# Performance work log

Hardware: AMD Instinct MI355X
Metric: run time of the kernel (lower is better)

The kernel has to match this reference:

```python
import jax, jax.numpy as jnp
import numpy as np

N = 50000      # nodes
E = 400000     # lower-adjacency edges (avg degree 8)
D = 128        # input_dim == output_dim (o_dim in DEC_HOGNN)
GEO = 20       # geo_dim
H = 3          # heads
C = 128        # out_channels per head
NUM_LAYERS = 3


def _lin_init(key, fan_in, fan_out, extra=()):
    s = 1.0 / np.sqrt(fan_in)
    return jax.random.uniform(key, extra + (fan_in, fan_out), jnp.float32, -s, s)


def setup_inputs() -> dict:
    key = jax.random.key(0)
    ks = jax.random.split(key, 20)
    inp = {
        "h": jax.random.normal(ks[0], (N, D), jnp.float32),
        "lower_adj_feat": jax.random.normal(ks[1], (E, GEO), jnp.float32),
        "dir_w": jax.random.normal(ks[2], (E, 1), jnp.float32),
        "src_idx": jax.random.randint(ks[3], (E,), 0, N),
        "dst_idx": jax.random.randint(ks[4], (E,), 0, N),
        # edge_encoder: Linear(2*D + geo + 1 -> D)
        "W_ee": _lin_init(ks[5], 2 * D + GEO + 1, D),
        "b_ee": jnp.zeros((D,), jnp.float32),
        # residual linear (layer 0 only; others Identity)
        "W_res": _lin_init(ks[6], D, D),
        "b_res": jnp.zeros((D,), jnp.float32),
        # 3 TransformerConv layers, all in=D out=C heads=H (stacked)
        "Wq": _lin_init(ks[7], D, H * C, (NUM_LAYERS,)),
        "bq": jnp.zeros((NUM_LAYERS, H * C), jnp.float32),
        "Wk": _lin_init(ks[8], D, H * C, (NUM_LAYERS,)),
        "bk": jnp.zeros((NUM_LAYERS, H * C), jnp.float32),
        "Wv": _lin_init(ks[9], D, H * C, (NUM_LAYERS,)),
        "bv": jnp.zeros((NUM_LAYERS, H * C), jnp.float32),
        "We": _lin_init(ks[10], D, H * C, (NUM_LAYERS,)),
        "be": jnp.zeros((NUM_LAYERS, H * C), jnp.float32),
        # lin_skip: in -> out_channels (concat=False)
        "Ws": _lin_init(ks[11], D, C, (NUM_LAYERS,)),
        "bs": jnp.zeros((NUM_LAYERS, C), jnp.float32),
        # ctr_lin: Linear(input_dim + output_dim -> output_dim)
        "W_ctr": _lin_init(ks[12], 2 * D, D),
        "b_ctr": jnp.zeros((D,), jnp.float32),
    }
    return inp


def _transformer_conv(x, src, dst, e_attr, Wq, bq, Wk, bk, Wv, bv, We, be, Ws, bs):
    """PyG TransformerConv, heads=H, concat=False (head mean), root skip."""
    n = x.shape[0]
    q = (x @ Wq + bq).reshape(n, H, C)
    k = (x @ Wk + bk).reshape(n, H, C)
    v = (x @ Wv + bv).reshape(n, H, C)
    e = (e_attr @ We + be).reshape(-1, H, C)      # [E,H,C]
    ke = k[src] + e                                # edge-conditioned keys
    alpha = (q[dst] * ke).sum(-1) / jnp.sqrt(jnp.asarray(C, x.dtype))  # [E,H]
    # segment softmax over destination nodes
    amax = jax.ops.segment_max(alpha, dst, num_segments=n)
    amax = jnp.where(jnp.isfinite(amax), amax, 0.0)
    ex = jnp.exp(alpha - amax[dst])
    den = jax.ops.segment_sum(ex, dst, num_segments=n)
    w = ex / (den[dst] + 1e-16)
    msg = (v[src] + e) * w[:, :, None]             # [E,H,C]
    out = jax.ops.segment_sum(msg.reshape(-1, H * C), dst, num_segments=n)
    out = out.reshape(n, H, C).mean(axis=1)        # concat=False -> head mean
    return out + x @ Ws + bs                       # root weight skip


def reference(h, lower_adj_feat, dir_w, src_idx, dst_idx,
              W_ee, b_ee, W_res, b_res,
              Wq, bq, Wk, bk, Wv, bv, We, be, Ws, bs,
              W_ctr, b_ctr):
    # edge encoder: [h[dst], h[src]*dir, dir, geo] -> D
    edge_features = jnp.concatenate(
        [h[dst_idx], h[src_idx] * dir_w, dir_w, lower_adj_feat], axis=-1)
    edge_attr = edge_features @ W_ee + b_ee
    h_cur = h
    for i in range(NUM_LAYERS):
        residual = (h_cur @ W_res + b_res) if i == 0 else h_cur
        h_t = _transformer_conv(h_cur, src_idx, dst_idx, edge_attr,
                                Wq[i], bq[i], Wk[i], bk[i], Wv[i], bv[i],
                                We[i], be[i], Ws[i], bs[i])
        h_cur = jax.nn.relu(h_t + residual)
    return jnp.concatenate([h, h_cur], axis=-1) @ W_ctr + b_ctr
```

## Files before the change

kernel.cpp:

```cpp
#include <hip/hip_runtime.h>
#include <math.h>

#define NN 50000
#define NE 400000

typedef _Float16 f16;
typedef _Float16 f16x8 __attribute__((ext_vector_type(8)));
typedef _Float16 f16x4 __attribute__((ext_vector_type(4)));
typedef _Float16 f16x2 __attribute__((ext_vector_type(2)));
typedef float f32x4 __attribute__((ext_vector_type(4)));

static __device__ __forceinline__ float dot8(f16x8 a, f16x8 b, float acc) {
#if defined(__has_builtin) && __has_builtin(__builtin_amdgcn_fdot2)
#pragma unroll
  for (int j = 0; j < 4; ++j) {
    f16x2 x = {a[2 * j], a[2 * j + 1]};
    f16x2 y = {b[2 * j], b[2 * j + 1]};
    acc = __builtin_amdgcn_fdot2(x, y, acc, false);
  }
#else
#pragma unroll
  for (int j = 0; j < 8; ++j) acc += (float)a[j] * (float)b[j];
#endif
  return acc;
}

#if defined(__has_builtin) && __has_builtin(__builtin_amdgcn_global_load_lds)
#define HAVE_GLL 1
static __device__ __forceinline__ void gload_lds16(const f16* gp, f16* lp) {
  __builtin_amdgcn_global_load_lds((const __attribute__((address_space(1))) void*)gp,
                                   (__attribute__((address_space(3))) void*)lp, 16, 0, 0);
}
#else
#define HAVE_GLL 0
#endif

__global__ __launch_bounds__(256) void hgemm_k128_kernel(
    const f16* __restrict__ A, int lda,
    const f16* __restrict__ WT,
    const float* __restrict__ bias,
    f16* __restrict__ outb, int ldb,
    int M, int ntiles)
{
  __shared__ f16 As[128 * 128];
  __shared__ f16 Bs[64 * 128];
  const int t = threadIdx.x;
  const int wv = t >> 6, lane = t & 63;
  const int l15 = lane & 15, l4 = lane >> 4;
  const int c8 = lane & 15, rsub = lane >> 4;
  const int row0 = blockIdx.x * 128;

#if HAVE_GLL
#pragma unroll
  for (int k = 0; k < 8; ++k) {
    int r = wv * 4 + k * 16 + rsub;
    int rc = row0 + r; if (rc >= M) rc = M - 1;
    const f16* gp = A + (size_t)rc * lda + ((c8 ^ (r & 15)) << 3);
    gload_lds16(gp, As + (wv * 4 + k * 16) * 128);
  }
#else
  for (int i = t; i < 2048; i += 256) {
    int r = i >> 4, cc = i & 15;
    int gr = row0 + r; if (gr >= M) gr = M - 1;
    float4 v = *(const float4*)(A + (size_t)gr * lda + cc * 8);
    *(float4*)(As + r * 128 + ((cc ^ (r & 15)) << 3)) = v;
  }
#endif
  for (int ct = 0; ct < ntiles; ++ct) {
    const int col0 = (blockIdx.y * ntiles + ct) * 64;
#if HAVE_GLL
#pragma unroll
    for (int k = 0; k < 4; ++k) {
      int c = wv * 4 + k * 16 + rsub;
      const f16* gp = WT + (size_t)(col0 + c) * 128 + ((c8 ^ (c & 15)) << 3);
      gload_lds16(gp, Bs + (wv * 4 + k * 16) * 128);
    }
#else
    for (int i = t; i < 1024; i += 256) {
      int c = i >> 4, cc = i & 15;
      float4 v = *(const float4*)(WT + (size_t)(col0 + c) * 128 + cc * 8);
      *(float4*)(Bs + c * 128 + ((cc ^ (c & 15)) << 3)) = v;
    }
#endif
    __syncthreads();
    f32x4 acc[2][4];
#pragma unroll
    for (int m = 0; m < 2; ++m)
#pragma unroll
      for (int n = 0; n < 4; ++n) acc[m][n] = (f32x4){0.f, 0.f, 0.f, 0.f};
#pragma unroll
    for (int ks = 0; ks < 4; ++ks) {
      const int co = (((ks * 4 + l4) ^ l15) << 3);
      f16x8 a0 = *(const f16x8*)(As + (wv * 32 +      l15) * 128 + co);
      f16x8 a1 = *(const f16x8*)(As + (wv * 32 + 16 + l15) * 128 + co);
      f16x8 b0 = *(const f16x8*)(Bs + (     l15) * 128 + co);
      f16x8 b1 = *(const f16x8*)(Bs + (16 + l15) * 128 + co);
      f16x8 b2 = *(const f16x8*)(Bs + (32 + l15) * 128 + co);
      f16x8 b3 = *(const f16x8*)(Bs + (48 + l15) * 128 + co);
      acc[0][0] = __builtin_amdgcn_mfma_f32_16x16x32_f16(a0, b0, acc[0][0], 0, 0, 0);
      acc[0][1] = __builtin_amdgcn_mfma_f32_16x16x32_f16(a0, b1, acc[0][1], 0, 0, 0);
      acc[0][2] = __builtin_amdgcn_mfma_f32_16x16x32_f16(a0, b2, acc[0][2], 0, 0, 0);
      acc[0][3] = __builtin_amdgcn_mfma_f32_16x16x32_f16(a0, b3, acc[0][3], 0, 0, 0);
      acc[1][0] = __builtin_amdgcn_mfma_f32_16x16x32_f16(a1, b0, acc[1][0], 0, 0, 0);
      acc[1][1] = __builtin_amdgcn_mfma_f32_16x16x32_f16(a1, b1, acc[1][1], 0, 0, 0);
      acc[1][2] = __builtin_amdgcn_mfma_f32_16x16x32_f16(a1, b2, acc[1][2], 0, 0, 0);
      acc[1][3] = __builtin_amdgcn_mfma_f32_16x16x32_f16(a1, b3, acc[1][3], 0, 0, 0);
    }
    __syncthreads();
    float bv4[4];
#pragma unroll
    for (int n = 0; n < 4; ++n) bv4[n] = bias ? bias[col0 + n * 16 + l15] : 0.f;
#pragma unroll
    for (int m = 0; m < 2; ++m) {
#pragma unroll
      for (int j = 0; j < 4; ++j) {
        int r = row0 + wv * 32 + m * 16 + l4 * 4 + j;
        if (r >= M) continue;
#pragma unroll
        for (int n = 0; n < 4; ++n) {
          int c = col0 + n * 16 + l15;
          outb[(size_t)r * ldb + c] = (f16)(acc[m][n][j] + bv4[n]);
        }
      }
    }
  }
}

__global__ __launch_bounds__(256) void pgemm_kernel(
    const f16* __restrict__ Abase, const f16* __restrict__ Wbase,
    f16* __restrict__ Obase, int mode)
{
  __shared__ f16 As[128 * 128];
  __shared__ f16 Bs[64 * 128];
  const int t = threadIdx.x;
  const int wv = t >> 6, lane = t & 63;
  const int l15 = lane & 15, l4 = lane >> 4;
  const int c8 = lane & 15, rsub = lane >> 4;
  const int row0 = blockIdx.x * 128;
  const int z = blockIdx.z;
  const f16* A; const f16* WT; int ldw, ntiles, ih = 0, hh = 0;
  f16* Os;
  if (mode == 0) {
    A = Abase; WT = Wbase + (size_t)z * 49152; ldw = 128;
    Os = Obase + (size_t)z * 147456; ntiles = 3;
  } else {
    ih = z / 3; hh = z % 3;
    A = Abase + (size_t)z * 49152;
    WT = Wbase + (size_t)ih * 49152 + hh * 128; ldw = 384;
    Os = Obase + (size_t)ih * 114688; ntiles = 1;
  }
#if HAVE_GLL
#pragma unroll
  for (int k = 0; k < 8; ++k) {
    int r = wv * 4 + k * 16 + rsub;
    const f16* gp = A + (size_t)(row0 + r) * 128 + ((c8 ^ (r & 15)) << 3);
    gload_lds16(gp, As + (wv * 4 + k * 16) * 128);
  }
#else
  for (int i = t; i < 2048; i += 256) {
    int r = i >> 4, cc = i & 15;
    float4 v = *(const float4*)(A + (size_t)(row0 + r) * 128 + cc * 8);
    *(float4*)(As + r * 128 + ((cc ^ (r & 15)) << 3)) = v;
  }
#endif
  for (int ct = 0; ct < ntiles; ++ct) {
    const int col0 = (blockIdx.y * ntiles + ct) * 64;
#if HAVE_GLL
#pragma unroll
    for (int k = 0; k < 4; ++k) {
      int c = wv * 4 + k * 16 + rsub;
      const f16* gp = WT + (size_t)(col0 + c) * ldw + ((c8 ^ (c & 15)) << 3);
      gload_lds16(gp, Bs + (wv * 4 + k * 16) * 128);
    }
#else
    for (int i = t; i < 1024; i += 256) {
      int c = i >> 4, cc = i & 15;
      float4 v = *(const float4*)(WT + (size_t)(col0 + c) * ldw + cc * 8);
      *(float4*)(Bs + c * 128 + ((cc ^ (c & 15)) << 3)) = v;
    }
#endif
    __syncthreads();
    f32x4 acc[2][4];
#pragma unroll
    for (int m = 0; m < 2; ++m)
#pragma unroll
      for (int n = 0; n < 4; ++n) acc[m][n] = (f32x4){0.f, 0.f, 0.f, 0.f};
#pragma unroll
    for (int ks = 0; ks < 4; ++ks) {
      const int co = (((ks * 4 + l4) ^ l15) << 3);
      f16x8 a0 = *(const f16x8*)(As + (wv * 32 +      l15) * 128 + co);
      f16x8 a1 = *(const f16x8*)(As + (wv * 32 + 16 + l15) * 128 + co);
      f16x8 b0 = *(const f16x8*)(Bs + (     l15) * 128 + co);
      f16x8 b1 = *(const f16x8*)(Bs + (16 + l15) * 128 + co);
      f16x8 b2 = *(const f16x8*)(Bs + (32 + l15) * 128 + co);
      f16x8 b3 = *(const f16x8*)(Bs + (48 + l15) * 128 + co);
      acc[0][0] = __builtin_amdgcn_mfma_f32_16x16x32_f16(a0, b0, acc[0][0], 0, 0, 0);
      acc[0][1] = __builtin_amdgcn_mfma_f32_16x16x32_f16(a0, b1, acc[0][1], 0, 0, 0);
      acc[0][2] = __builtin_amdgcn_mfma_f32_16x16x32_f16(a0, b2, acc[0][2], 0, 0, 0);
      acc[0][3] = __builtin_amdgcn_mfma_f32_16x16x32_f16(a0, b3, acc[0][3], 0, 0, 0);
      acc[1][0] = __builtin_amdgcn_mfma_f32_16x16x32_f16(a1, b0, acc[1][0], 0, 0, 0);
      acc[1][1] = __builtin_amdgcn_mfma_f32_16x16x32_f16(a1, b1, acc[1][1], 0, 0, 0);
      acc[1][2] = __builtin_amdgcn_mfma_f32_16x16x32_f16(a1, b2, acc[1][2], 0, 0, 0);
      acc[1][3] = __builtin_amdgcn_mfma_f32_16x16x32_f16(a1, b3, acc[1][3], 0, 0, 0);
    }
    __syncthreads();
#pragma unroll
    for (int m = 0; m < 2; ++m) {
#pragma unroll
      for (int j = 0; j < 4; ++j) {
        int r = row0 + wv * 32 + m * 16 + l4 * 4 + j;
#pragma unroll
        for (int n = 0; n < 4; ++n) {
          int cc = col0 + n * 16 + l15;
          f16 v = (f16)acc[m][n][j];
          if (mode == 0) {
            Os[(size_t)r * 384 + cc] = v;
          } else if (r < 280) {
            int c;
            if (r < 128)      c = hh * 128 + r;
            else if (r < 256) c = 384 + hh * 128 + (r - 128);
            else              c = 768 + hh * 24 + (r - 256);
            Os[(size_t)c * 128 + cc] = v;
          }
        }
      }
    }
  }
}

__global__ __launch_bounds__(256) void hgemm2_kernel(
    const f16* __restrict__ A, int lda,
    const f16* __restrict__ A2, int lda2, int a2k,
    const f16* __restrict__ WT, int K,
    const float* __restrict__ bias,
    f16* __restrict__ outb, int ldb,
    const f16* __restrict__ fresid, int ldr,
    int dorelu, int M,
    const f16* __restrict__ ctrW, const float* __restrict__ ctrB,
    float* __restrict__ ctrOut)
{
  __shared__ f16 As[128 * 128];
  __shared__ f16 Bs[128 * 128];
  const int t = threadIdx.x;
  const int wv = t >> 6, lane = t & 63;
  const int l15 = lane & 15, l4 = lane >> 4;
  const int c8 = lane & 15, rsub = lane >> 4;
  const int row0 = blockIdx.x * 128;
  const int col0 = blockIdx.y * 128;

  f32x4 acc[2][8];
#pragma unroll
  for (int m = 0; m < 2; ++m)
#pragma unroll
    for (int n = 0; n < 8; ++n) acc[m][n] = (f32x4){0.f, 0.f, 0.f, 0.f};

  for (int kc = 0; kc < K; kc += 128) {
    const f16* Ap; int koff, ldA;
    if (kc >= a2k) { Ap = A2; koff = kc - a2k; ldA = lda2; }
    else           { Ap = A;  koff = kc;       ldA = lda;  }
#if HAVE_GLL
#pragma unroll
    for (int k = 0; k < 8; ++k) {
      int r = wv * 4 + k * 16 + rsub;
      int rc = row0 + r; if (rc >= M) rc = M - 1;
      const f16* gp = Ap + (size_t)rc * ldA + koff + ((c8 ^ (r & 15)) << 3);
      gload_lds16(gp, As + (wv * 4 + k * 16) * 128);
    }
#pragma unroll
    for (int k = 0; k < 8; ++k) {
      int c = wv * 4 + k * 16 + rsub;
      const f16* gp = WT + (size_t)(col0 + c) * K + kc + ((c8 ^ (c & 15)) << 3);
      gload_lds16(gp, Bs + (wv * 4 + k * 16) * 128);
    }
#else
    for (int i = t; i < 2048; i += 256) {
      int r = i >> 4, cc = i & 15;
      int gr = row0 + r; if (gr >= M) gr = M - 1;
      float4 v = *(const float4*)(Ap + (size_t)gr * ldA + koff + cc * 8);
      *(float4*)(As + r * 128 + ((cc ^ (r & 15)) << 3)) = v;
    }
    for (int i = t; i < 2048; i += 256) {
      int c = i >> 4, cc = i & 15;
      float4 v = *(const float4*)(WT + (size_t)(col0 + c) * K + kc + cc * 8);
      *(float4*)(Bs + c * 128 + ((cc ^ (c & 15)) << 3)) = v;
    }
#endif
    __syncthreads();
#pragma unroll
    for (int ks = 0; ks < 4; ++ks) {
      const int co = (((ks * 4 + l4) ^ l15) << 3);
      f16x8 a0 = *(const f16x8*)(As + (wv * 32 +      l15) * 128 + co);
      f16x8 a1 = *(const f16x8*)(As + (wv * 32 + 16 + l15) * 128 + co);
#pragma unroll
      for (int n = 0; n < 8; ++n) {
        f16x8 b = *(const f16x8*)(Bs + (n * 16 + l15) * 128 + co);
        acc[0][n] = __builtin_amdgcn_mfma_f32_16x16x32_f16(a0, b, acc[0][n], 0, 0, 0);
        acc[1][n] = __builtin_amdgcn_mfma_f32_16x16x32_f16(a1, b, acc[1][n], 0, 0, 0);
      }
    }
    __syncthreads();
  }

  float bv8[8];
#pragma unroll
  for (int n = 0; n < 8; ++n) bv8[n] = bias ? bias[col0 + n * 16 + l15] : 0.f;
#pragma unroll
  for (int m = 0; m < 2; ++m) {
#pragma unroll
    for (int j = 0; j < 4; ++j) {
      int rl = wv * 32 + m * 16 + l4 * 4 + j;
      int r = row0 + rl;
#pragma unroll
      for (int n = 0; n < 8; ++n) {
        int c = col0 + n * 16 + l15;
        float val = acc[m][n][j] + bv8[n];
        if (fresid) val += (float)fresid[(size_t)r * ldr + c];
        if (dorelu) val = fmaxf(val, 0.f);
        f16 hv = (f16)val;
        if (r < M) outb[(size_t)r * ldb + c] = hv;
        if (ctrOut)
          As[rl * 128 + (((c >> 3) ^ (rl & 15)) << 3) + (c & 7)] = hv;
      }
    }
  }

  if (ctrOut) {
    for (int i = t; i < 2048; i += 256) {
      int c = i >> 4, k8 = i & 15;
      float4 v = *(const float4*)(ctrW + (size_t)c * 256 + k8 * 8);
      *(float4*)(Bs + c * 128 + ((k8 ^ (c & 15)) << 3)) = v;
    }
    __syncthreads();
    f32x4 acc2[2][8];
#pragma unroll
    for (int m = 0; m < 2; ++m)
#pragma unroll
      for (int n = 0; n < 8; ++n) acc2[m][n] = (f32x4){0.f, 0.f, 0.f, 0.f};
#pragma unroll
    for (int ks = 0; ks < 4; ++ks) {
      const int co = (((ks * 4 + l4) ^ l15) << 3);
      f16x8 a0 = *(const f16x8*)(As + (wv * 32 +      l15) * 128 + co);
      f16x8 a1 = *(const f16x8*)(As + (wv * 32 + 16 + l15) * 128 + co);
#pragma unroll
      for (int n = 0; n < 8; ++n) {
        f16x8 b = *(const f16x8*)(Bs + (n * 16 + l15) * 128 + co);
        acc2[0][n] = __builtin_amdgcn_mfma_f32_16x16x32_f16(a0, b, acc2[0][n], 0, 0, 0);
        acc2[1][n] = __builtin_amdgcn_mfma_f32_16x16x32_f16(a1, b, acc2[1][n], 0, 0, 0);
      }
    }
    __syncthreads();
    for (int i = t; i < 2048; i += 256) {
      int r = i >> 4, k8 = i & 15;
      int gr = row0 + r; if (gr >= M) gr = M - 1;
      float4 v = *(const float4*)(A2 + (size_t)gr * lda2 + 128 + k8 * 8);
      *(float4*)(As + r * 128 + ((k8 ^ (r & 15)) << 3)) = v;
    }
    for (int i = t; i < 2048; i += 256) {
      int c = i >> 4, k8 = i & 15;
      float4 v = *(const float4*)(ctrW + (size_t)c * 256 + 128 + k8 * 8);
      *(float4*)(Bs + c * 128 + ((k8 ^ (c & 15)) << 3)) = v;
    }
    __syncthreads();
#pragma unroll
    for (int ks = 0; ks < 4; ++ks) {
      const int co = (((ks * 4 + l4) ^ l15) << 3);
      f16x8 a0 = *(const f16x8*)(As + (wv * 32 +      l15) * 128 + co);
      f16x8 a1 = *(const f16x8*)(As + (wv * 32 + 16 + l15) * 128 + co);
#pragma unroll
      for (int n = 0; n < 8; ++n) {
        f16x8 b = *(const f16x8*)(Bs + (n * 16 + l15) * 128 + co);
        acc2[0][n] = __builtin_amdgcn_mfma_f32_16x16x32_f16(a0, b, acc2[0][n], 0, 0, 0);
        acc2[1][n] = __builtin_amdgcn_mfma_f32_16x16x32_f16(a1, b, acc2[1][n], 0, 0, 0);
      }
    }
#pragma unroll
    for (int m = 0; m < 2; ++m) {
#pragma unroll
      for (int j = 0; j < 4; ++j) {
        int r = row0 + wv * 32 + m * 16 + l4 * 4 + j;
        if (r >= M) continue;
#pragma unroll
        for (int n = 0; n < 8; ++n) {
          int c = n * 16 + l15;
          ctrOut[(size_t)r * 128 + c] = acc2[m][n][j] + ctrB[c];
        }
      }
    }
  }
}

__global__ void zero_int_kernel(int* __restrict__ p, int n) {
  int i = blockIdx.x * 256 + threadIdx.x;
  if (i < n) p[i] = 0;
}
__global__ void hist_kernel(const int* __restrict__ dst, int* __restrict__ deg) {
  int e = blockIdx.x * 256 + threadIdx.x;
  if (e < NE) atomicAdd(&deg[dst[e]], 1);
}
__global__ void scanA_kernel(const int* __restrict__ deg, int* __restrict__ rowstart,
                             int* __restrict__ part) {
  __shared__ int sd[256];
  int b = blockIdx.x, t = threadIdx.x, i = b * 256 + t;
  sd[t] = (i < NN) ? deg[i] : 0;
  __syncthreads();
  for (int o = 1; o < 256; o <<= 1) {
    int v = (t >= o) ? sd[t - o] : 0;
    __syncthreads();
    sd[t] += v;
    __syncthreads();
  }
  if (i < NN) rowstart[i + 1] = sd[t];
  if (t == 255) part[b] = sd[255];
}
__global__ void scanB_kernel(int* __restrict__ part, int nb) {
  __shared__ int sd[256];
  int t = threadIdx.x;
  sd[t] = (t < nb) ? part[t] : 0;
  __syncthreads();
  for (int o = 1; o < 256; o <<= 1) {
    int v = (t >= o) ? sd[t - o] : 0;
    __syncthreads();
    sd[t] += v;
    __syncthreads();
  }
  if (t < nb) part[t] = sd[t];
}
__global__ void scanC_kernel(const int* __restrict__ deg, int* __restrict__ rowstart,
                             const int* __restrict__ part, int* __restrict__ cursor) {
  int b = blockIdx.x, t = threadIdx.x, i = b * 256 + t;
  if (i >= NN) return;
  int off = b ? part[b - 1] : 0;
  int fin = rowstart[i + 1] + off;
  rowstart[i + 1] = fin;
  cursor[i] = fin - deg[i];
  if (i == 0) rowstart[0] = 0;
}
__global__ void scatter_kernel(const int* __restrict__ dst, const int* __restrict__ src,
                               const float* __restrict__ dirw, const float* __restrict__ geo,
                               int* __restrict__ cursor,
                               int* __restrict__ srcp, f16* __restrict__ dirpb,
                               f16* __restrict__ geop) {
  int e = blockIdx.x * 256 + threadIdx.x;
  if (e < NE) {
    int pos = atomicAdd(&cursor[dst[e]], 1);
    srcp[pos] = src[e];
    float dv = dirw[e];
    dirpb[pos] = (f16)dv;
    f16* gp = geop + (size_t)pos * 24;
#pragma unroll
    for (int j = 0; j < 20; ++j) gp[j] = (f16)geo[(size_t)e * 20 + j];
    gp[20] = (f16)dv;
    gp[21] = (f16)0.f; gp[22] = (f16)0.f; gp[23] = (f16)0.f;
  }
}

__global__ void convert_kernel(const float* __restrict__ Wee, const float* __restrict__ bee,
                               const float* __restrict__ WeAll, const float* __restrict__ Wq,
                               const float* __restrict__ Wk,
                               f16* __restrict__ Vf, f16* __restrict__ WeT,
                               f16* __restrict__ Wq16, f16* __restrict__ Wk16)
{
  int idx = blockIdx.x * 256 + threadIdx.x;
  if (idx < 49152) {
    int r = idx >> 7, j = idx & 127;
    float v = 0.f;
    if (r < 128)       v = Wee[(size_t)(128 + r) * 128 + j];
    else if (r < 256)  v = Wee[(size_t)(r - 128) * 128 + j];
    else if (r < 276)  v = Wee[(size_t)(257 + (r - 256)) * 128 + j];
    else if (r == 276) v = Wee[(size_t)256 * 128 + j];
    else if (r == 277) v = bee[j];
    Vf[idx] = (f16)v;
  } else if (idx < 196608) {
    int rr = idx - 49152; int i = rr / 49152; int r2 = rr % 49152;
    int cc = r2 >> 7, j = r2 & 127;
    WeT[rr] = (f16)WeAll[((size_t)i * 128 + j) * 384 + cc];
  } else if (idx < 344064) {
    int rr = idx - 196608;
    Wq16[rr] = (f16)Wq[rr];
  } else if (idx < 491520) {
    int rr = idx - 344064;
    Wk16[rr] = (f16)Wk[rr];
  }
}

__global__ void arows_kernel(const f16* __restrict__ Wk16, const f16* __restrict__ Sall,
                             f16* __restrict__ Arows)
{
  int idx = blockIdx.x * 256 + threadIdx.x;
  if (idx >= 442368) return;
  int z = idx / 49152; int rr = idx % 49152; int r = rr >> 7; int k2 = rr & 127;
  int i = z / 3, h = z % 3;
  f16 v = (f16)0.f;
  if (r < 128)       v = Wk16[(size_t)i * 49152 + (size_t)r * 384 + h * 128 + k2];
  else if (r < 256)  v = Sall[(size_t)i * 147456 + (size_t)(r - 128) * 384 + h * 128 + k2];
  else if (r < 277)  v = Sall[(size_t)i * 147456 + (size_t)r * 384 + h * 128 + k2];
  Arows[idx] = v;
}

__global__ void biasAB_kernel(const f16* __restrict__ Arows, const float* __restrict__ bq,
                              float* __restrict__ biasAB)
{
  int idx = blockIdx.x * 256 + threadIdx.x;
  if (idx >= 2688) return;
  int i = idx / 896, c = idx % 896;
  float acc = 0.f;
  int h = 0, ro = -1;
  if (c < 384)      { h = c >> 7;         ro = c & 127; }
  else if (c < 768) { h = (c - 384) >> 7; ro = 128 + ((c - 384) & 127); }
  else if (c < 840) { h = (c - 768) / 24; ro = 256 + ((c - 768) % 24); }
  if (ro >= 0) {
    const f16* ar = Arows + ((size_t)(i * 3 + h)) * 49152 + (size_t)ro * 128;
    const float* bqh = bq + i * 384 + h * 128;
    for (int k2 = 0; k2 < 128; ++k2) acc += (float)ar[k2] * bqh[k2];
  }
  biasAB[idx] = acc;
}

__global__ void prep2_kernel(const f16* __restrict__ Sall, const float* __restrict__ beAll,
                             const float* __restrict__ Wv, const float* __restrict__ bv,
                             const float* __restrict__ Ws, const float* __restrict__ Wres,
                             f16* __restrict__ W2bigT)
{
  int idx = blockIdx.x * 256 + threadIdx.x;
  if (idx >= 442368) return;
  int i = idx / 147456; int r = idx % 147456; int c = r / 1152; int k = r % 1152;
  const f16* S = Sall + (size_t)i * 147456;
  float v = 0.f;
  if (k < 384) {
    int h = k >> 7, tt = k & 127;
    v = (float)S[(size_t)tt * 384 + h * 128 + c];
  } else if (k < 768) {
    int h = (k - 384) >> 7, u = (k - 384) & 127;
    v = Wv[((size_t)i * 128 + u) * 384 + h * 128 + c];
  } else if (k < 840) {
    int h = (k - 768) / 24, tt = (k - 768) % 24;
    if (tt < 21)       v = (float)S[(size_t)(256 + tt) * 384 + h * 128 + c];
    else if (tt == 21) v = (float)S[(size_t)277 * 384 + h * 128 + c]
                         + beAll[i * 384 + h * 128 + c] + bv[i * 384 + h * 128 + c];
  } else if (k < 896) {
    v = 0.f;
  } else if (k < 1024) {
    int tt = k - 896;
    v = ((float)S[(size_t)(128 + tt) * 384 + c]
       + (float)S[(size_t)(128 + tt) * 384 + 128 + c]
       + (float)S[(size_t)(128 + tt) * 384 + 256 + c]) * (1.0f / 3.0f);
  } else {
    v = Ws[((size_t)i * 128 + (k - 1024)) * 128 + c];
    if (i == 0) v += Wres[(k - 1024) * 128 + c];
  }
  W2bigT[(size_t)i * 147456 + c * 1152 + k] = (f16)v;
}

__global__ void wprep_kernel(const float* __restrict__ Wctr, const float* __restrict__ bs,
                             const float* __restrict__ bres,
                             f16* __restrict__ WctrT2, float* __restrict__ bias0)
{
  int idx = blockIdx.x * 256 + threadIdx.x;
  if (idx < 32768) {
    int c = idx >> 8, k = idx & 255;
    float v = (k < 128) ? Wctr[(size_t)(128 + k) * 128 + c]
                        : Wctr[(size_t)(k - 128) * 128 + c];
    WctrT2[idx] = (f16)v;
  } else if (idx < 32896) {
    int c = idx - 32768;
    bias0[c] = bs[c] + bres[c];
  }
}

__global__ __launch_bounds__(256) void attn_kernel(
    const f16* __restrict__ xh,
    f16* __restrict__ nbuf,
    const int* __restrict__ rowstart,
    const int* __restrict__ srcp,
    const f16* __restrict__ dirpb,
    const f16* __restrict__ geop)
{
  const int sl = threadIdx.x & 15;
  const int n = blockIdx.x * 16 + (threadIdx.x >> 4);
  const float rsC = 0.088388347648318447f;
  f16* row = nbuf + (size_t)n * 1024;

  f16x8 qk[3], g2[3];
#pragma unroll
  for (int h = 0; h < 3; ++h) {
    qk[h] = *(const f16x8*)(row + h * 128 + sl * 8);
    g2[h] = *(const f16x8*)(row + 384 + h * 128 + sl * 8);
  }
  float g34a[3], g34c[3];
#pragma unroll
  for (int h = 0; h < 3; ++h) {
    g34a[h] = (float)row[768 + h * 24 + sl];
    g34c[h] = (sl < 8) ? (float)row[768 + h * 24 + 16 + sl] : 0.f;
  }
  float den[3] = {0.f, 0.f, 0.f};
  float F2[3][8], Fv[3][8];
#pragma unroll
  for (int h = 0; h < 3; ++h)
#pragma unroll
    for (int j = 0; j < 8; ++j) { F2[h][j] = 0.f; Fv[h][j] = 0.f; }
  float f34a[3] = {0.f, 0.f, 0.f}, f34c[3] = {0.f, 0.f, 0.f};

  const int beg = rowstart[n], end = rowstart[n + 1];
  int ii = beg;
  for (; ii + 1 < end; ii += 2) {
    const int s0 = srcp[ii], s1 = srcp[ii + 1];
    const float d0 = (float)dirpb[ii], d1 = (float)dirpb[ii + 1];
    const f16* p0 = xh + (size_t)s0 * 256 + sl * 8;
    const f16* p1 = xh + (size_t)s1 * 256 + sl * 8;
    f16x8 xv0 = *(const f16x8*)p0;
    f16x8 hv0 = *(const f16x8*)(p0 + 128);
    f16x8 xv1 = *(const f16x8*)p1;
    f16x8 hv1 = *(const f16x8*)(p1 + 128);
    const float gea0 = (float)geop[(size_t)ii * 24 + sl];
    const float geb0 = (sl < 8) ? (float)geop[(size_t)ii * 24 + 16 + sl] : 0.f;
    const float gea1 = (float)geop[(size_t)(ii + 1) * 24 + sl];
    const float geb1 = (sl < 8) ? (float)geop[(size_t)(ii + 1) * 24 + 16 + sl] : 0.f;

    float pa[6];
#pragma unroll
    for (int h = 0; h < 3; ++h) {
      pa[h]     = dot8(qk[h], xv0, 0.f) + d0 * dot8(g2[h], hv0, 0.f)
                + gea0 * g34a[h] + geb0 * g34c[h];
      pa[3 + h] = dot8(qk[h], xv1, 0.f) + d1 * dot8(g2[h], hv1, 0.f)
                + gea1 * g34a[h] + geb1 * g34c[h];
    }
#pragma unroll
    for (int off = 1; off < 16; off <<= 1) {
#pragma unroll
      for (int q = 0; q < 6; ++q) pa[q] += __shfl_xor(pa[q], off);
    }
    float w0[3], w1[3];
#pragma unroll
    for (int h = 0; h < 3; ++h) {
      w0[h] = __expf(pa[h] * rsC);
      w1[h] = __expf(pa[3 + h] * rsC);
      den[h] += w0[h] + w1[h];
    }
#pragma unroll
    for (int h = 0; h < 3; ++h) {
      const float wd0 = w0[h] * d0, wd1 = w1[h] * d1;
#pragma unroll
      for (int j = 0; j < 8; ++j) {
        F2[h][j] = fmaf(wd0, (float)hv0[j], fmaf(wd1, (float)hv1[j], F2[h][j]));
        Fv[h][j] = fmaf(w0[h], (float)xv0[j], fmaf(w1[h], (float)xv1[j], Fv[h][j]));
      }
      f34a[h] = fmaf(w0[h], gea0, fmaf(w1[h], gea1, f34a[h]));
      f34c[h] = fmaf(w0[h], geb0, fmaf(w1[h], geb1, f34c[h]));
    }
  }
  if (ii < end) {
    const int s0 = srcp[ii];
    const float d0 = (float)dirpb[ii];
    const f16* p0 = xh + (size_t)s0 * 256 + sl * 8;
    f16x8 xv0 = *(const f16x8*)p0;
    f16x8 hv0 = *(const f16x8*)(p0 + 128);
    const float gea0 = (float)geop[(size_t)ii * 24 + sl];
    const float geb0 = (sl < 8) ? (float)geop[(size_t)ii * 24 + 16 + sl] : 0.f;
    float pa[3];
#pragma unroll
    for (int h = 0; h < 3; ++h)
      pa[h] = dot8(qk[h], xv0, 0.f) + d0 * dot8(g2[h], hv0, 0.f)
            + gea0 * g34a[h] + geb0 * g34c[h];
#pragma unroll
    for (int off = 1; off < 16; off <<= 1) {
#pragma unroll
      for (int q = 0; q < 3; ++q) pa[q] += __shfl_xor(pa[q], off);
    }
#pragma unroll
    for (int h = 0; h < 3; ++h) {
      const float w = __expf(pa[h] * rsC);
      den[h] += w;
      const float wd = w * d0;
#pragma unroll
      for (int j = 0; j < 8; ++j) {
        F2[h][j] = fmaf(wd, (float)hv0[j], F2[h][j]);
        Fv[h][j] = fmaf(w, (float)xv0[j], Fv[h][j]);
      }
      f34a[h] = fmaf(w, gea0, f34a[h]);
      f34c[h] = fmaf(w, geb0, f34c[h]);
    }
  }

  float sc[3], swh[3];
#pragma unroll
  for (int h = 0; h < 3; ++h) {
    sc[h] = (1.f / 3.f) / (den[h] + 1e-16f);
    swh[h] = den[h] * sc[h];
  }
#pragma unroll
  for (int h = 0; h < 3; ++h) {
    f16x8 o1, o2;
#pragma unroll
    for (int j = 0; j < 8; ++j) {
      o1[j] = (f16)(F2[h][j] * sc[h]);
      o2[j] = (f16)(Fv[h][j] * sc[h]);
    }
    *(f16x8*)(row + h * 128 + sl * 8) = o1;
    *(f16x8*)(row + 384 + h * 128 + sl * 8) = o2;
  }
#pragma unroll
  for (int h = 0; h < 3; ++h) {
    row[768 + h * 24 + sl] = (f16)(f34a[h] * sc[h]);
    if (sl < 8) {
      float fcv = (sl == 5) ? swh[h] : f34c[h] * sc[h];
      row[768 + h * 24 + 16 + sl] = (f16)fcv;
    }
  }
  f16x8 ho = *(const f16x8*)(xh + (size_t)n * 256 + 128 + sl * 8);
  if (beg >= end) {
#pragma unroll
    for (int j = 0; j < 8; ++j) ho[j] = (f16)0.f;
  }
  *(f16x8*)(row + 896 + sl * 8) = ho;
}

__global__ void hconv_kernel(const float* __restrict__ src, f16* __restrict__ xh) {
  int i = blockIdx.x * 256 + threadIdx.x;
  if (i >= NN * 32) return;
  float4 a = ((const float4*)src)[i];
  f16x4 o;
  o[0] = (f16)a.x; o[1] = (f16)a.y; o[2] = (f16)a.z; o[3] = (f16)a.w;
  int r = i >> 5, c4 = i & 31;
  *(f16x4*)(xh + (size_t)r * 256 + c4 * 4) = o;
  *(f16x4*)(xh + (size_t)r * 256 + 128 + c4 * 4) = o;
}

extern "C" void kernel_launch(void* const* d_in, const int* in_sizes, int n_in,
                              void* d_out, int out_size, void* d_ws, size_t ws_size,
                              hipStream_t stream)
{
  (void)in_sizes; (void)n_in; (void)out_size; (void)ws_size;
  const float* h    = (const float*)d_in[0];
  const float* geo  = (const float*)d_in[1];
  const float* dirw = (const float*)d_in[2];
  const int*   src  = (const int*)d_in[3];
  const int*   dst  = (const int*)d_in[4];
  const float* Wee  = (const float*)d_in[5];
  const float* bee  = (const float*)d_in[6];
  const float* Wres = (const float*)d_in[7];
  const float* bres = (const float*)d_in[8];
  const float* Wq   = (const float*)d_in[9];
  const float* bq   = (const float*)d_in[10];
  const float* Wk   = (const float*)d_in[11];
  const float* bk   = (const float*)d_in[12];  (void)bk;
  const float* Wv   = (const float*)d_in[13];
  const float* bv   = (const float*)d_in[14];
  const float* We   = (const float*)d_in[15];
  const float* be   = (const float*)d_in[16];
  const float* Ws   = (const float*)d_in[17];
  const float* bs   = (const float*)d_in[18];
  const float* Wctr = (const float*)d_in[19];
  const float* bctr = (const float*)d_in[20];

  char* base = (char*)d_ws;
  size_t off = 0;
  auto take = [&](size_t bytes) -> char* {
    char* p = base + off;
    off += bytes;
    off = (off + 255) & ~(size_t)255;
    return p;
  };
  f16* nbuf     = (f16*)take((size_t)NN * 1024 * 2);
  f16* xh       = (f16*)take((size_t)NN * 256 * 2);
  f16* Vf16     = (f16*)take(49152 * 2);
  f16* WeT16    = (f16*)take((size_t)3 * 49152 * 2);
  f16* Wq16     = (f16*)take((size_t)3 * 49152 * 2);
  f16* Wk16     = (f16*)take((size_t)3 * 49152 * 2);
  f16* Sall     = (f16*)take((size_t)3 * 147456 * 2);
  f16* Arows    = (f16*)take((size_t)9 * 49152 * 2);
  f16* WABT     = (f16*)take((size_t)3 * 114688 * 2);
  float* biasAB = (float*)take((size_t)3 * 896 * 4);
  f16* W2bigT   = (f16*)take((size_t)3 * 147456 * 2);
  f16* WctrT2   = (f16*)take(32768 * 2);
  float* bias0  = (float*)take(128 * 4);
  f16* dirpb    = (f16*)take((size_t)NE * 2);
  f16* geop     = (f16*)take((size_t)NE * 24 * 2);
  int* deg      = (int*)take((size_t)NN * 4);
  int* rowstart = (int*)take((size_t)(NN + 1) * 4);
  int* cursor   = (int*)take((size_t)NN * 4);
  int* srcp     = (int*)take((size_t)NE * 4);
  int* part     = (int*)take(256 * 4);

  zero_int_kernel<<<(NN + 255) / 256, 256, 0, stream>>>(deg, NN);
  hist_kernel<<<(NE + 255) / 256, 256, 0, stream>>>(dst, deg);
  scanA_kernel<<<196, 256, 0, stream>>>(deg, rowstart, part);
  scanB_kernel<<<1, 256, 0, stream>>>(part, 196);
  scanC_kernel<<<196, 256, 0, stream>>>(deg, rowstart, part, cursor);
  scatter_kernel<<<(NE + 255) / 256, 256, 0, stream>>>(dst, src, dirw, geo, cursor,
                                                       srcp, dirpb, geop);
  hconv_kernel<<<6250, 256, 0, stream>>>(h, xh);
  wprep_kernel<<<129, 256, 0, stream>>>(Wctr, bs, bres, WctrT2, bias0);

  convert_kernel<<<(491520 + 255) / 256, 256, 0, stream>>>(Wee, bee, We, Wq, Wk,
                                                           Vf16, WeT16, Wq16, Wk16);
  pgemm_kernel<<<dim3(3, 2, 3), 256, 0, stream>>>(Vf16, WeT16, Sall, 0);
  arows_kernel<<<(442368 + 255) / 256, 256, 0, stream>>>(Wk16, Sall, Arows);
  pgemm_kernel<<<dim3(3, 2, 9), 256, 0, stream>>>(Arows, Wq16, WABT, 1);
  biasAB_kernel<<<11, 256, 0, stream>>>(Arows, bq, biasAB);
  prep2_kernel<<<(442368 + 255) / 256, 256, 0, stream>>>(Sall, be, Wv, bv, Ws, Wres, W2bigT);

  for (int i = 0; i < 3; ++i) {
    hgemm_k128_kernel<<<dim3(391, 2), 256, 0, stream>>>(xh, 256, WABT + (size_t)i * 114688,
        biasAB + (size_t)i * 896, nbuf, 1024, NN, 7);
    attn_kernel<<<3125, 256, 0, stream>>>(xh, nbuf, rowstart, srcp, dirpb, geop);
    const float* obias = (i == 0) ? bias0 : (bs + i * 128);
    const f16* resid = (i == 0) ? nullptr : xh;
    const f16* ctrW = (i == 2) ? WctrT2 : nullptr;
    const float* ctrB = (i == 2) ? bctr : nullptr;
    float* ctrOut = (i == 2) ? (float*)d_out : nullptr;
    hgemm2_kernel<<<dim3(391, 1), 256, 0, stream>>>(nbuf, 1024, xh, 256, 1024,
        W2bigT + (size_t)i * 147456, 1152, obias, xh, 256,
        resid, 256, 1, NN, ctrW, ctrB, ctrOut);
  }
}
```

Baseline: 569.6 us.

## Fuse next-layer projection GEMM into hgemm2 epilogue and merge prep kernels

The hgemm2 epilogue now keeps the freshly computed node features in shared memory and immediately multiplies them by the next layer's WABT weights, in 14 chunks of 64 columns, writing the 896-column projection into nbuf. This removes the separate per-layer hgemm_k128 launch and its re-read of xh; only the first layer's projection is still launched on its own. Several small setup kernels (arows, prep2, biasAB, hconv, wprep) are also merged into two combined launches to cut launch overhead. The trade-off is that the 896 projection columns are computed serially inside 391 blocks, instead of spread across the 782 blocks of the old standalone GEMM, which lengthens each hgemm2 block.

```diff
diff --git a/kernel.cpp b/kernel.cpp
--- a/kernel.cpp
+++ b/kernel.cpp
@@ -237,7 +237,9 @@
     const f16* __restrict__ fresid, int ldr,
     int dorelu, int M,
     const f16* __restrict__ ctrW, const float* __restrict__ ctrB,
-    float* __restrict__ ctrOut)
+    float* __restrict__ ctrOut,
+    const f16* __restrict__ fatW, const float* __restrict__ fatB,
+    f16* __restrict__ fatOut)
 {
   __shared__ f16 As[128 * 128];
   __shared__ f16 Bs[128 * 128];
@@ -301,6 +303,7 @@
     __syncthreads();
   }
 
+  const bool stash = (ctrOut != nullptr) || (fatOut != nullptr);
   float bv8[8];
 #pragma unroll
   for (int n = 0; n < 8; ++n) bv8[n] = bias ? bias[col0 + n * 16 + l15] : 0.f;
@@ -318,7 +321,7 @@
         if (dorelu) val = fmaxf(val, 0.f);
         f16 hv = (f16)val;
         if (r < M) outb[(size_t)r * ldb + c] = hv;
-        if (ctrOut)
+        if (stash)
           As[rl * 128 + (((c >> 3) ^ (rl & 15)) << 3) + (c & 7)] = hv;
       }
     }
@@ -385,6 +388,55 @@
           ctrOut[(size_t)r * 128 + c] = acc2[m][n][j] + ctrB[c];
         }
       }
+    }
+  }
+
+  if (fatOut) {
+    for (int ct = 0; ct < 14; ++ct) {
+      const int cf0 = ct * 64;
+      for (int i = t; i < 1024; i += 256) {
+        int c = i >> 4, k8 = i & 15;
+        float4 v = *(const float4*)(fatW + (size_t)(cf0 + c) * 128 + k8 * 8);
+        *(float4*)(Bs + c * 128 + ((k8 ^ (c & 15)) << 3)) = v;
+      }
+      __syncthreads();
+      f32x4 acc3[2][4];
+#pragma unroll
+      for (int m = 0; m < 2; ++m)
+#pragma unroll
+        for (int n = 0; n < 4; ++n) acc3[m][n] = (f32x4){0.f, 0.f, 0.f, 0.f};
+#pragma unroll
+      for (int ks = 0; ks < 4; ++ks) {
+        const int co = (((ks * 4 + l4) ^ l15) << 3);
+        f16x8 a0 = *(const f16x8*)(As + (wv * 32 +      l15) * 128 + co);
+        f16x8 a1 = *(const f16x8*)(As + (wv * 32 + 16 + l15) * 128 + co);
+        f16x8 b0 = *(const f16x8*)(Bs + (     l15) * 128 + co);
+        f16x8 b1 = *(const f16x8*)(Bs + (16 + l15) * 128 + co);
+        f16x8 b2 = *(const f16x8*)(Bs + (32 + l15) * 128 + co);
+        f16x8 b3 = *(const f16x8*)(Bs + (48 + l15) * 128 + co);
+        acc3[0][0] = __builtin_amdgcn_mfma_f32_16x16x32_f16(a0, b0, acc3[0][0], 0, 0, 0);
+        acc3[0][1] = __builtin_amdgcn_mfma_f32_16x16x32_f16(a0, b1, acc3[0][1], 0, 0, 0);
+        acc3[0][2] = __builtin_amdgcn_mfma_f32_16x16x32_f16(a0, b2, acc3[0][2], 0, 0, 0);
+        acc3[0][3] = __builtin_amdgcn_mfma_f32_16x16x32_f16(a0, b3, acc3[0][3], 0, 0, 0);
+        acc3[1][0] = __builtin_amdgcn_mfma_f32_16x16x32_f16(a1, b0, acc3[1][0], 0, 0, 0);
+        acc3[1][1] = __builtin_amdgcn_mfma_f32_16x16x32_f16(a1, b1, acc3[1][1], 0, 0, 0);
+        acc3[1][2] = __builtin_amdgcn_mfma_f32_16x16x32_f16(a1, b2, acc3[1][2], 0, 0, 0);
+        acc3[1][3] = __builtin_amdgcn_mfma_f32_16x16x32_f16(a1, b3, acc3[1][3], 0, 0, 0);
+      }
+#pragma unroll
+      for (int m = 0; m < 2; ++m) {
+#pragma unroll
+        for (int j = 0; j < 4; ++j) {
+          int r = row0 + wv * 32 + m * 16 + l4 * 4 + j;
+          if (r >= M) continue;
+#pragma unroll
+          for (int n = 0; n < 4; ++n) {
+            int c = cf0 + n * 16 + l15;
+            fatOut[(size_t)r * 1024 + c] = (f16)(acc3[m][n][j] + fatB[c]);
+          }
+        }
+      }
+      __syncthreads();
     }
   }
 }
@@ -483,86 +535,87 @@
   }
 }
 
-__global__ void arows_kernel(const f16* __restrict__ Wk16, const f16* __restrict__ Sall,
-                             f16* __restrict__ Arows)
+__global__ void postS_kernel(const f16* __restrict__ Wk16, const f16* __restrict__ Sall,
+                             const float* __restrict__ beAll, const float* __restrict__ Wv,
+                             const float* __restrict__ bv, const float* __restrict__ Ws,
+                             const float* __restrict__ Wres, const float* __restrict__ bq,
+                             f16* __restrict__ Arows, f16* __restrict__ W2bigT,
+                             float* __restrict__ biasAB)
 {
   int idx = blockIdx.x * 256 + threadIdx.x;
-  if (idx >= 442368) return;
-  int z = idx / 49152; int rr = idx % 49152; int r = rr >> 7; int k2 = rr & 127;
-  int i = z / 3, h = z % 3;
-  f16 v = (f16)0.f;
-  if (r < 128)       v = Wk16[(size_t)i * 49152 + (size_t)r * 384 + h * 128 + k2];
-  else if (r < 256)  v = Sall[(size_t)i * 147456 + (size_t)(r - 128) * 384 + h * 128 + k2];
-  else if (r < 277)  v = Sall[(size_t)i * 147456 + (size_t)r * 384 + h * 128 + k2];
-  Arows[idx] = v;
-}
-
-__global__ void biasAB_kernel(const f16* __restrict__ Arows, const float* __restrict__ bq,
-                              float* __restrict__ biasAB)
+  if (idx < 442368) {
+    int z = idx / 49152; int rr = idx % 49152; int r = rr >> 7; int k2 = rr & 127;
+    int i = z / 3, h = z % 3;
+    f16 v = (f16)0.f;
+    if (r < 128)       v = Wk16[(size_t)i * 49152 + (size_t)r * 384 + h * 128 + k2];
+    else if (r < 256)  v = Sall[(size_t)i * 147456 + (size_t)(r - 128) * 384 + h * 128 + k2];
+    else if (r < 277)  v = Sall[(size_t)i * 147456 + (size_t)r * 384 + h * 128 + k2];
+    Arows[idx] = v;
+  } else if (idx < 884736) {
+    int r0 = idx - 442368;
+    int i = r0 / 147456; int r = r0 % 147456; int c = r / 1152; int k = r % 1152;
+    const f16* S = Sall + (size_t)i * 147456;
+    float v = 0.f;
+    if (k < 384) {
+      int h = k >> 7, tt = k & 127;
+      v = (float)S[(size_t)tt * 384 + h * 128 + c];
+    } else if (k < 768) {
+      int h = (k - 384) >> 7, u = (k - 384) & 127;
+      v = Wv[((size_t)i * 128 + u) * 384 + h * 128 + c];
+    } else if (k < 840) {
+      int h = (k - 768) / 24, tt = (k - 768) % 24;
+      if (tt < 21)       v = (float)S[(size_t)(256 + tt) * 384 + h * 128 + c];
+      else if (tt == 21) v = (float)S[(size_t)277 * 384 + h * 128 + c]
+                           + beAll[i * 384 + h * 128 + c] + bv[i * 384 + h * 128 + c];
+    } else if (k < 896) {
+      v = 0.f;
+    } else if (k < 1024) {
+      int tt = k - 896;
+      v = ((float)S[(size_t)(128 + tt) * 384 + c]
+         + (float)S[(size_t)(128 + tt) * 384 + 128 + c]
+         + (float)S[(size_t)(128 + tt) * 384 + 256 + c]) * (1.0f / 3.0f);
+    } else {
+      v = Ws[((size_t)i * 128 + (k - 1024)) * 128 + c];
+      if (i == 0) v += Wres[(k - 1024) * 128 + c];
+    }
+    W2bigT[(size_t)i * 147456 + c * 1152 + k] = (f16)v;
+  } else if (idx < 887424) {
+    int r = idx - 884736; int i = r / 896; int c = r % 896;
+    float acc = 0.f;
+    int h = 0, ro = -1;
+    if (c < 384)      { h = c >> 7;         ro = c & 127; }
+    else if (c < 768) { h = (c - 384) >> 7; ro = 128 + ((c - 384) & 127); }
+    else if (c < 840) { h = (c - 768) / 24; ro = 256 + ((c - 768) % 24); }
+    if (ro >= 0) {
+      const f16* ar = Arows + ((size_t)(i * 3 + h)) * 49152 + (size_t)ro * 128;
+      const float* bqh = bq + i * 384 + h * 128;
+      for (int k2 = 0; k2 < 128; ++k2) acc += (float)ar[k2] * bqh[k2];
+    }
+    biasAB[r] = acc;
+  }
+}
+
+__global__ void misc_kernel(const float* __restrict__ src, f16* __restrict__ xh,
+                            const float* __restrict__ Wctr, const float* __restrict__ bs,
+                            const float* __restrict__ bres,
+                            f16* __restrict__ WctrT2, float* __restrict__ bias0)
 {
   int idx = blockIdx.x * 256 + threadIdx.x;
-  if (idx >= 2688) return;
-  int i = idx / 896, c = idx % 896;
-  float acc = 0.f;
-  int h = 0, ro = -1;
-  if (c < 384)      { h = c >> 7;         ro = c & 127; }
-  else if (c < 768) { h = (c - 384) >> 7; ro = 128 + ((c - 384) & 127); }
-  else if (c < 840) { h = (c - 768) / 24; ro = 256 + ((c - 768) % 24); }
-  if (ro >= 0) {
-    const f16* ar = Arows + ((size_t)(i * 3 + h)) * 49152 + (size_t)ro * 128;
-    const float* bqh = bq + i * 384 + h * 128;
-    for (int k2 = 0; k2 < 128; ++k2) acc += (float)ar[k2] * bqh[k2];
-  }
-  biasAB[idx] = acc;
-}
-
-__global__ void prep2_kernel(const f16* __restrict__ Sall, const float* __restrict__ beAll,
-                             const float* __restrict__ Wv, const float* __restrict__ bv,
-                             const float* __restrict__ Ws, const float* __restrict__ Wres,
-                             f16* __restrict__ W2bigT)
-{
-  int idx = blockIdx.x * 256 + threadIdx.x;
-  if (idx >= 442368) return;
-  int i = idx / 147456; int r = idx % 147456; int c = r / 1152; int k = r % 1152;
-  const f16* S = Sall + (size_t)i * 147456;
-  float v = 0.f;
-  if (k < 384) {
-    int h = k >> 7, tt = k & 127;
-    v = (float)S[(size_t)tt * 384 + h * 128 + c];
-  } else if (k < 768) {
-    int h = (k - 384) >> 7, u = (k - 384) & 127;
-    v = Wv[((size_t)i * 128 + u) * 384 + h * 128 + c];
-  } else if (k < 840) {
-    int h = (k - 768) / 24, tt = (k - 768) % 24;
-    if (tt < 21)       v = (float)S[(size_t)(256 + tt) * 384 + h * 128 + c];
-    else if (tt == 21) v = (float)S[(size_t)277 * 384 + h * 128 + c]
-                         + beAll[i * 384 + h * 128 + c] + bv[i * 384 + h * 128 + c];
-  } else if (k < 896) {
-    v = 0.f;
-  } else if (k < 1024) {
-    int tt = k - 896;
-    v = ((float)S[(size_t)(128 + tt) * 384 + c]
-       + (float)S[(size_t)(128 + tt) * 384 + 128 + c]
-       + (float)S[(size_t)(128 + tt) * 384 + 256 + c]) * (1.0f / 3.0f);
-  } else {
-    v = Ws[((size_t)i * 128 + (k - 1024)) * 128 + c];
-    if (i == 0) v += Wres[(k - 1024) * 128 + c];
-  }
-  W2bigT[(size_t)i * 147456 + c * 1152 + k] = (f16)v;
-}
-
-__global__ void wprep_kernel(const float* __restrict__ Wctr, const float* __restrict__ bs,
-                             const float* __restrict__ bres,
-                             f16* __restrict__ WctrT2, float* __restrict__ bias0)
-{
-  int idx = blockIdx.x * 256 + threadIdx.x;
-  if (idx < 32768) {
-    int c = idx >> 8, k = idx & 255;
+  if (idx < NN * 32) {
+    float4 a = ((const float4*)src)[idx];
+    f16x4 o;
+    o[0] = (f16)a.x; o[1] = (f16)a.y; o[2] = (f16)a.z; o[3] = (f16)a.w;
+    int r = idx >> 5, c4 = idx & 31;
+    *(f16x4*)(xh + (size_t)r * 256 + c4 * 4) = o;
+    *(f16x4*)(xh + (size_t)r * 256 + 128 + c4 * 4) = o;
+  } else if (idx < NN * 32 + 32768) {
+    int r = idx - NN * 32;
+    int c = r >> 8, k = r & 255;
     float v = (k < 128) ? Wctr[(size_t)(128 + k) * 128 + c]
                         : Wctr[(size_t)(k - 128) * 128 + c];
-    WctrT2[idx] = (f16)v;
-  } else if (idx < 32896) {
-    int c = idx - 32768;
+    WctrT2[r] = (f16)v;
+  } else if (idx < NN * 32 + 32896) {
+    int c = idx - NN * 32 - 32768;
     bias0[c] = bs[c] + bres[c];
   }
 }
@@ -712,17 +765,6 @@
     for (int j = 0; j < 8; ++j) ho[j] = (f16)0.f;
   }
   *(f16x8*)(row + 896 + sl * 8) = ho;
-}
-
-__global__ void hconv_kernel(const float* __restrict__ src, f16* __restrict__ xh) {
-  int i = blockIdx.x * 256 + threadIdx.x;
-  if (i >= NN * 32) return;
-  float4 a = ((const float4*)src)[i];
-  f16x4 o;
-  o[0] = (f16)a.x; o[1] = (f16)a.y; o[2] = (f16)a.z; o[3] = (f16)a.w;
-  int r = i >> 5, c4 = i & 31;
-  *(f16x4*)(xh + (size_t)r * 256 + c4 * 4) = o;
-  *(f16x4*)(xh + (size_t)r * 256 + 128 + c4 * 4) = o;
 }
 
 extern "C" void kernel_launch(void* const* d_in, const int* in_sizes, int n_in,
@@ -788,28 +830,29 @@
   scanC_kernel<<<196, 256, 0, stream>>>(deg, rowstart, part, cursor);
   scatter_kernel<<<(NE + 255) / 256, 256, 0, stream>>>(dst, src, dirw, geo, cursor,
                                                        srcp, dirpb, geop);
-  hconv_kernel<<<6250, 256, 0, stream>>>(h, xh);
-  wprep_kernel<<<129, 256, 0, stream>>>(Wctr, bs, bres, WctrT2, bias0);
-
+  misc_kernel<<<(NN * 32 + 32896 + 255) / 256, 256, 0, stream>>>(h, xh, Wctr, bs, bres,
+                                                                 WctrT2, bias0);
   convert_kernel<<<(491520 + 255) / 256, 256, 0, stream>>>(Wee, bee, We, Wq, Wk,
                                                            Vf16, WeT16, Wq16, Wk16);
   pgemm_kernel<<<dim3(3, 2, 3), 256, 0, stream>>>(Vf16, WeT16, Sall, 0);
-  arows_kernel<<<(442368 + 255) / 256, 256, 0, stream>>>(Wk16, Sall, Arows);
+  postS_kernel<<<(887424 + 255) / 256, 256, 0, stream>>>(Wk16, Sall, be, Wv, bv, Ws,
+                                                         Wres, bq, Arows, W2bigT, biasAB);
   pgemm_kernel<<<dim3(3, 2, 9), 256, 0, stream>>>(Arows, Wq16, WABT, 1);
-  biasAB_kernel<<<11, 256, 0, stream>>>(Arows, bq, biasAB);
-  prep2_kernel<<<(442368 + 255) / 256, 256, 0, stream>>>(Sall, be, Wv, bv, Ws, Wres, W2bigT);
+
+  hgemm_k128_kernel<<<dim3(391, 2), 256, 0, stream>>>(xh, 256, WABT, biasAB, nbuf, 1024, NN, 7);
 
   for (int i = 0; i < 3; ++i) {
-    hgemm_k128_kernel<<<dim3(391, 2), 256, 0, stream>>>(xh, 256, WABT + (size_t)i * 114688,
-        biasAB + (size_t)i * 896, nbuf, 1024, NN, 7);
     attn_kernel<<<3125, 256, 0, stream>>>(xh, nbuf, rowstart, srcp, dirpb, geop);
     const float* obias = (i == 0) ? bias0 : (bs + i * 128);
     const f16* resid = (i == 0) ? nullptr : xh;
     const f16* ctrW = (i == 2) ? WctrT2 : nullptr;
     const float* ctrB = (i == 2) ? bctr : nullptr;
     float* ctrOut = (i == 2) ? (float*)d_out : nullptr;
+    const f16* fatW = (i < 2) ? (WABT + (size_t)(i + 1) * 114688) : nullptr;
+    const float* fatB = (i < 2) ? (biasAB + (size_t)(i + 1) * 896) : nullptr;
+    f16* fatOut = (i < 2) ? nbuf : nullptr;
     hgemm2_kernel<<<dim3(391, 1), 256, 0, stream>>>(nbuf, 1024, xh, 256, 1024,
         W2bigT + (size_t)i * 147456, 1152, obias, xh, 256,
-        resid, 256, 1, NN, ctrW, ctrB, ctrOut);
-  }
-}
+        resid, 256, 1, NN, ctrW, ctrB, ctrOut, fatW, fatB, fatOut);
+  }
+}
```

Result: slower. 592.4 us (+4.0%).
